# Kernel tuning notes

Measured on AMD Instinct MI355X. Metric: run time of the kernel, lower is better.

The kernel has to match this reference:

```python
import jax, jax.numpy as jnp
import numpy as np

B, S, H, D = 8, 4096, 4096, 128
N_MAX = 64          # max_rope_sentences
THETA = 10000.0     # rope_theta
N_SENT = 40         # random sentence ends per sample (+1 forced at last token)


def setup_inputs() -> dict:
    key = jax.random.key(0)
    k0, k1, k2, k3 = jax.random.split(key, 4)
    hidden_states = jax.random.normal(k0, (B, S, H), jnp.float32)
    # sentence-end mask: N_SENT random positions per row + last token always an end
    m = np.zeros((B, S), np.int32)
    for i in range(B):
        pos = np.random.RandomState(i).choice(S - 1, N_SENT, replace=False)
        m[i, pos] = 1
    m[:, -1] = 1
    splitted_mask = jnp.asarray(m)
    scale = 1.0 / np.sqrt(H).astype(np.float32)
    Wq = jax.random.normal(k1, (H, D), jnp.float32) * scale
    Wk = jax.random.normal(k2, (H, D), jnp.float32) * scale
    Wr = jax.random.normal(k3, (H, 1), jnp.float32) * scale
    bq = jnp.zeros((D,), jnp.float32)
    bk = jnp.zeros((D,), jnp.float32)
    br = jnp.zeros((1,), jnp.float32)
    return dict(hidden_states=hidden_states, splitted_mask=splitted_mask,
                Wq=Wq, bq=bq, Wk=Wk, bk=bk, Wr=Wr, br=br)


def _rope(x, cos, sin):
    # x: [B, N, D]; interleaved complex pairs (even=real, odd=imag)
    a, b = x[..., 0::2], x[..., 1::2]
    ra = a * cos - b * sin
    rb = a * sin + b * cos
    return jnp.stack([ra, rb], axis=-1).reshape(x.shape)


def _rewards(hidden_states, splitted_mask, Wq, bq, Wk, bk, Wr, br):
    q_all = hidden_states @ Wq + bq                     # [B,S,D]
    k_all = hidden_states @ Wk + bk                     # [B,S,D]
    v_all = (hidden_states @ Wr + br)[..., 0]           # [B,S]

    mask = splitted_mask > 0                            # [B,S]
    count = mask.sum(axis=1)                            # [B], >=1 by construction
    rank = jnp.cumsum(mask, axis=1) - 1                 # sentence rank per position
    rank = jnp.where(mask, rank, N_MAX)                 # out-of-range -> dropped
    pos = jnp.broadcast_to(jnp.arange(S), (B, S))
    sent_pos = jnp.zeros((B, N_MAX), jnp.int32).at[
        jnp.arange(B)[:, None], rank].set(pos, mode='drop')   # [B,N_MAX]

    vs = jnp.take_along_axis(v_all, sent_pos, axis=1)               # [B,N]
    qs = jnp.take_along_axis(q_all, sent_pos[..., None], axis=1)    # [B,N,D]
    ks = jnp.take_along_axis(k_all, sent_pos[..., None], axis=1)    # [B,N,D]

    # RoPE over sentence rank 0..N_MAX-1
    freqs = 1.0 / (THETA ** (jnp.arange(0, D, 2, dtype=jnp.float32) / D))
    ang = jnp.arange(N_MAX, dtype=jnp.float32)[:, None] * freqs[None, :]
    cos, sin = jnp.cos(ang)[None], jnp.sin(ang)[None]   # [1,N,D/2]
    qs = _rope(qs, cos, sin)
    ks = _rope(ks, cos, sin)

    # query = rotated q of the LAST sentence in each sample
    seq_q = jnp.take_along_axis(qs, (count - 1)[:, None, None], axis=1)[:, 0]  # [B,D]

    # sentence rewards: first = vs[0], rest = successive diffs
    sr = vs - jnp.pad(vs[:, :-1], ((0, 0), (1, 0)))     # [B,N]

    logits = jnp.einsum('bd,bnd->bn', seq_q, ks) / jnp.sqrt(jnp.float32(D))
    valid = jnp.arange(N_MAX)[None, :] < count[:, None]
    logits = jnp.where(valid, logits, -jnp.inf)
    attn = jax.nn.softmax(logits, axis=-1)              # [B,N]
    seq_reward = jnp.sum(attn * sr, axis=-1)            # [B]
    return seq_reward


def reference(hidden_states, splitted_mask, Wq, bq, Wk, bk, Wr, br):
    rewards = _rewards(hidden_states, splitted_mask, Wq, bq, Wk, bk, Wr, br)
    bs = B // 2
    chosen, reject = rewards[:bs], rewards[bs:]
    loss = jnp.mean(-jax.nn.log_sigmoid(chosen - reject))  # penalty_coef = 0
    return loss, rewards
```

## Files before the change

### kernel.cpp

```cpp
#include <hip/hip_runtime.h>
#include <math.h>

#define BB 8
#define SS 4096
#define HH 4096
#define DD 128
#define NMAX 64

__global__ void scan_kernel(const int* __restrict__ mask,
                            int* __restrict__ sent_pos,
                            int* __restrict__ count) {
    int b = blockIdx.x;
    int lane = threadIdx.x;
    int running = 0;
    const int* mrow = mask + (size_t)b * SS;
    for (int base = 0; base < SS; base += 64) {
        int m = (mrow[base + lane] > 0) ? 1 : 0;
        unsigned long long bal = __ballot(m);
        if (m) {
            int r = running + __popcll(bal & ((1ull << lane) - 1ull));
            if (r < NMAX) sent_pos[b * NMAX + r] = base + lane;
        }
        running += __popcll(bal);
    }
    if (lane == 0) count[b] = running > NMAX ? NMAX : running;
}

__global__ void proj_kernel(const float* __restrict__ hs,
                            const float* __restrict__ Wq, const float* __restrict__ bq,
                            const float* __restrict__ Wk, const float* __restrict__ bk,
                            const float* __restrict__ Wr, const float* __restrict__ br,
                            const int* __restrict__ sent_pos, const int* __restrict__ count,
                            float* __restrict__ qrow,
                            float* __restrict__ krows,
                            float* __restrict__ vs) {
    int b = blockIdx.y;
    int j = blockIdx.x;
    int tid = threadIdx.x;
    bool is_q = (j == NMAX);
    int cnt = count[b];
    if (!is_q && j >= cnt) return;

    int row = is_q ? (SS - 1) : sent_pos[b * NMAX + j];
    const float* x = hs + ((size_t)b * SS + (size_t)row) * HH;

    __shared__ float xs[HH];
    __shared__ float4 red[256];
    __shared__ float vred[256];

    for (int i = tid; i < HH / 4; i += 256)
        ((float4*)xs)[i] = ((const float4*)x)[i];
    __syncthreads();

    const float* W = is_q ? Wq : Wk;
    const float* bias = is_q ? bq : bk;

    int d0 = (tid & 31) * 4;
    int h0 = (tid >> 5) * (HH / 8);
    const float* Wp = W + (size_t)h0 * DD + d0;
    float4 acc = make_float4(0.f, 0.f, 0.f, 0.f);
#pragma unroll 4
    for (int h = 0; h < HH / 8; ++h) {
        float xv = xs[h0 + h];
        float4 w = *(const float4*)Wp;
        Wp += DD;
        acc.x += xv * w.x;
        acc.y += xv * w.y;
        acc.z += xv * w.z;
        acc.w += xv * w.w;
    }
    red[tid] = acc;
    __syncthreads();

    if (tid < 32) {
        float4 s = red[tid];
#pragma unroll
        for (int p = 1; p < 8; ++p) {
            float4 o = red[tid + p * 32];
            s.x += o.x; s.y += o.y; s.z += o.z; s.w += o.w;
        }
        int dd = tid * 4;
        float* outp = is_q ? (qrow + b * DD) : (krows + ((size_t)b * NMAX + j) * DD);
        outp[dd + 0] = s.x + bias[dd + 0];
        outp[dd + 1] = s.y + bias[dd + 1];
        outp[dd + 2] = s.z + bias[dd + 2];
        outp[dd + 3] = s.w + bias[dd + 3];
    }

    if (!is_q) {
        float pv = 0.f;
        for (int h = tid; h < HH; h += 256) pv += xs[h] * Wr[h];
        vred[tid] = pv;
        __syncthreads();
        for (int s = 128; s > 0; s >>= 1) {
            if (tid < s) vred[tid] += vred[tid + s];
            __syncthreads();
        }
        if (tid == 0) vs[b * NMAX + j] = vred[0] + br[0];
    }
}

__global__ void finalize_kernel(const float* __restrict__ qrow,
                                const float* __restrict__ krows,
                                const float* __restrict__ vs,
                                const int* __restrict__ count,
                                float* __restrict__ out) {
    __shared__ float sfreq[64];
    __shared__ float qr[BB][DD];
    __shared__ float rew[BB];

    int tid = threadIdx.x;
    if (tid < 64) sfreq[tid] = powf(10000.f, -(float)tid / 64.f);
    __syncthreads();

    int b = tid >> 6;
    int l = tid & 63;
    int cnt = count[b];

    {
        float2 qp = ((const float2*)(qrow + b * DD))[l];
        float s, c;
        sincosf((float)(cnt - 1) * sfreq[l], &s, &c);
        qr[b][2 * l]     = qp.x * c - qp.y * s;
        qr[b][2 * l + 1] = qp.x * s + qp.y * c;
    }
    __syncthreads();

    float lg = -INFINITY;
    if (l < cnt) {
        const float2* kp = (const float2*)(krows + ((size_t)b * NMAX + l) * DD);
        float acc = 0.f;
#pragma unroll 8
        for (int i = 0; i < 64; ++i) {
            float2 kv = kp[i];
            float s, c;
            sincosf((float)l * sfreq[i], &s, &c);
            float kr0 = kv.x * c - kv.y * s;
            float kr1 = kv.x * s + kv.y * c;
            acc += qr[b][2 * i] * kr0 + qr[b][2 * i + 1] * kr1;
        }
        lg = acc * 0.08838834764831845f;
    }

    float m = lg;
#pragma unroll
    for (int off = 32; off > 0; off >>= 1) m = fmaxf(m, __shfl_xor(m, off));
    float e = expf(lg - m);
    float sum = e;
#pragma unroll
    for (int off = 32; off > 0; off >>= 1) sum += __shfl_xor(sum, off);
    float attn = e / sum;

    float vn = 0.f, vp = 0.f;
    if (l < cnt) {
        vn = vs[b * NMAX + l];
        if (l > 0) vp = vs[b * NMAX + l - 1];
    }
    float r = attn * (vn - vp);
#pragma unroll
    for (int off = 32; off > 0; off >>= 1) r += __shfl_xor(r, off);

    if (l == 0) {
        rew[b] = r;
        out[1 + b] = r;
    }
    __syncthreads();

    if (tid == 0) {
        float L = 0.f;
        for (int i = 0; i < BB / 2; ++i) {
            float z = rew[i] - rew[i + BB / 2];
            L += fmaxf(-z, 0.f) + log1pf(expf(-fabsf(z)));
        }
        out[0] = L / (float)(BB / 2);
    }
}

extern "C" void kernel_launch(void* const* d_in, const int* in_sizes, int n_in,
                              void* d_out, int out_size, void* d_ws, size_t ws_size,
                              hipStream_t stream) {
    const float* hs  = (const float*)d_in[0];
    const int*   msk = (const int*)d_in[1];
    const float* Wq  = (const float*)d_in[2];
    const float* bq  = (const float*)d_in[3];
    const float* Wk  = (const float*)d_in[4];
    const float* bk  = (const float*)d_in[5];
    const float* Wr  = (const float*)d_in[6];
    const float* br  = (const float*)d_in[7];
    float* out = (float*)d_out;

    int* sent_pos = (int*)d_ws;
    int* count    = sent_pos + BB * NMAX;
    float* qrow   = (float*)(count + 8);
    float* krows  = qrow + BB * DD;
    float* vsbuf  = krows + (size_t)BB * NMAX * DD;

    scan_kernel<<<BB, 64, 0, stream>>>(msk, sent_pos, count);
    proj_kernel<<<dim3(NMAX + 1, BB), 256, 0, stream>>>(
        hs, Wq, bq, Wk, bk, Wr, br, sent_pos, count, qrow, krows, vsbuf);
    finalize_kernel<<<1, 512, 0, stream>>>(qrow, krows, vsbuf, count, out);
}
```

Baseline: 687.8 us.

## Batch eight gathered rows per block and split hidden dim with atomic accumulation

The projection kernel now handles eight sentence rows per block, so each weight float4 loaded from Wq/Wk is reused across eight rows instead of one. The hidden dimension is also split into four slices across blockIdx.z, and partial sums are combined with atomicAdd into outputs that are first initialised with the biases. The scan kernel becomes a 256-thread block prefix sum using vectorised mask loads. This cuts the repeated streaming of the 2 MB weight matrices per row and adds parallelism, at the cost of float atomics, which make the summation order nondeterministic, and more registers for the eight accumulators.

```diff
diff --git a/kernel.cpp b/kernel.cpp
--- a/kernel.cpp
+++ b/kernel.cpp
@@ -6,97 +6,160 @@
 #define HH 4096
 #define DD 128
 #define NMAX 64
+#define RPB 8
+#define HSL 1024
 
 __global__ void scan_kernel(const int* __restrict__ mask,
+                            const float* __restrict__ bq,
+                            const float* __restrict__ bk,
+                            const float* __restrict__ br,
                             int* __restrict__ sent_pos,
-                            int* __restrict__ count) {
-    int b = blockIdx.x;
-    int lane = threadIdx.x;
-    int running = 0;
-    const int* mrow = mask + (size_t)b * SS;
-    for (int base = 0; base < SS; base += 64) {
-        int m = (mrow[base + lane] > 0) ? 1 : 0;
-        unsigned long long bal = __ballot(m);
-        if (m) {
-            int r = running + __popcll(bal & ((1ull << lane) - 1ull));
-            if (r < NMAX) sent_pos[b * NMAX + r] = base + lane;
-        }
-        running += __popcll(bal);
-    }
-    if (lane == 0) count[b] = running > NMAX ? NMAX : running;
-}
-
-__global__ void proj_kernel(const float* __restrict__ hs,
-                            const float* __restrict__ Wq, const float* __restrict__ bq,
-                            const float* __restrict__ Wk, const float* __restrict__ bk,
-                            const float* __restrict__ Wr, const float* __restrict__ br,
-                            const int* __restrict__ sent_pos, const int* __restrict__ count,
+                            int* __restrict__ count,
                             float* __restrict__ qrow,
                             float* __restrict__ krows,
                             float* __restrict__ vs) {
+    int b = blockIdx.x;
+    int t = threadIdx.x;
+
+    for (int i = t; i < DD; i += 256) qrow[b * DD + i] = bq[i];
+    for (int i = t; i < NMAX * DD; i += 256) krows[b * NMAX * DD + i] = bk[i & (DD - 1)];
+    if (t < NMAX) vs[b * NMAX + t] = br[0];
+
+    const int4* m4 = (const int4*)(mask + (size_t)b * SS);
+    int vals[16];
+    {
+        int4 v0 = m4[t * 4 + 0], v1 = m4[t * 4 + 1], v2 = m4[t * 4 + 2], v3 = m4[t * 4 + 3];
+        vals[0] = v0.x; vals[1] = v0.y; vals[2] = v0.z; vals[3] = v0.w;
+        vals[4] = v1.x; vals[5] = v1.y; vals[6] = v1.z; vals[7] = v1.w;
+        vals[8] = v2.x; vals[9] = v2.y; vals[10] = v2.z; vals[11] = v2.w;
+        vals[12] = v3.x; vals[13] = v3.y; vals[14] = v3.z; vals[15] = v3.w;
+    }
+    int c = 0;
+#pragma unroll
+    for (int i = 0; i < 16; ++i) c += (vals[i] > 0) ? 1 : 0;
+
+    __shared__ int sc[256];
+    sc[t] = c;
+    __syncthreads();
+    for (int off = 1; off < 256; off <<= 1) {
+        int add = (t >= off) ? sc[t - off] : 0;
+        __syncthreads();
+        sc[t] += add;
+        __syncthreads();
+    }
+    int prefix = sc[t] - c;
+    int total = sc[255];
+
+    int r = prefix;
+#pragma unroll
+    for (int i = 0; i < 16; ++i) {
+        if (vals[i] > 0) {
+            if (r < NMAX) sent_pos[b * NMAX + r] = t * 16 + i;
+            r++;
+        }
+    }
+    if (t == 0) count[b] = total > NMAX ? NMAX : total;
+}
+
+__global__ void __launch_bounds__(256)
+proj_kernel(const float* __restrict__ hs,
+            const float* __restrict__ Wq,
+            const float* __restrict__ Wk,
+            const float* __restrict__ Wr,
+            const int* __restrict__ sent_pos, const int* __restrict__ count,
+            float* __restrict__ qrow,
+            float* __restrict__ krows,
+            float* __restrict__ vs) {
+    int g = blockIdx.x;
     int b = blockIdx.y;
-    int j = blockIdx.x;
-    int tid = threadIdx.x;
-    bool is_q = (j == NMAX);
+    int s = blockIdx.z;
+    int t = threadIdx.x;
     int cnt = count[b];
-    if (!is_q && j >= cnt) return;
-
-    int row = is_q ? (SS - 1) : sent_pos[b * NMAX + j];
-    const float* x = hs + ((size_t)b * SS + (size_t)row) * HH;
-
-    __shared__ float xs[HH];
-    __shared__ float4 red[256];
-    __shared__ float vred[256];
-
-    for (int i = tid; i < HH / 4; i += 256)
-        ((float4*)xs)[i] = ((const float4*)x)[i];
-    __syncthreads();
-
-    const float* W = is_q ? Wq : Wk;
-    const float* bias = is_q ? bq : bk;
-
-    int d0 = (tid & 31) * 4;
-    int h0 = (tid >> 5) * (HH / 8);
-    const float* Wp = W + (size_t)h0 * DD + d0;
-    float4 acc = make_float4(0.f, 0.f, 0.f, 0.f);
-#pragma unroll 4
-    for (int h = 0; h < HH / 8; ++h) {
-        float xv = xs[h0 + h];
-        float4 w = *(const float4*)Wp;
-        Wp += DD;
-        acc.x += xv * w.x;
-        acc.y += xv * w.y;
-        acc.z += xv * w.z;
-        acc.w += xv * w.w;
-    }
-    red[tid] = acc;
-    __syncthreads();
-
-    if (tid < 32) {
-        float4 s = red[tid];
-#pragma unroll
-        for (int p = 1; p < 8; ++p) {
-            float4 o = red[tid + p * 32];
-            s.x += o.x; s.y += o.y; s.z += o.z; s.w += o.w;
-        }
-        int dd = tid * 4;
-        float* outp = is_q ? (qrow + b * DD) : (krows + ((size_t)b * NMAX + j) * DD);
-        outp[dd + 0] = s.x + bias[dd + 0];
-        outp[dd + 1] = s.y + bias[dd + 1];
-        outp[dd + 2] = s.z + bias[dd + 2];
-        outp[dd + 3] = s.w + bias[dd + 3];
-    }
-
-    if (!is_q) {
-        float pv = 0.f;
-        for (int h = tid; h < HH; h += 256) pv += xs[h] * Wr[h];
-        vred[tid] = pv;
-        __syncthreads();
-        for (int s = 128; s > 0; s >>= 1) {
-            if (tid < s) vred[tid] += vred[tid + s];
-            __syncthreads();
-        }
-        if (tid == 0) vs[b * NMAX + j] = vred[0] + br[0];
+    int slot0 = g * RPB;
+    bool is_q_grp = (g == 8);
+    if (!is_q_grp && slot0 >= cnt) return;
+
+    int hoff = s * HSL;
+
+    __shared__ float xs[RPB][HSL];
+    __shared__ float wsum[RPB][4];
+
+    int wv = t >> 6;
+    int lane = t & 63;
+
+    float4 wr = ((const float4*)(Wr + hoff))[t];
+
+    for (int r = 0; r < RPB; ++r) {
+        int slot = slot0 + r;
+        bool valid = is_q_grp ? (r == 0) : (slot < cnt);
+        int row = is_q_grp ? (SS - 1) : (valid ? sent_pos[b * NMAX + slot] : 0);
+        float4 xv = make_float4(0.f, 0.f, 0.f, 0.f);
+        if (valid) {
+            const float4* xp = (const float4*)(hs + ((size_t)b * SS + (size_t)row) * HH + hoff);
+            xv = xp[t];
+        }
+        ((float4*)xs[r])[t] = xv;
+        if (!is_q_grp) {
+            float d = xv.x * wr.x + xv.y * wr.y + xv.z * wr.z + xv.w * wr.w;
+#pragma unroll
+            for (int off = 32; off > 0; off >>= 1) d += __shfl_down(d, off);
+            if (lane == 0) wsum[r][wv] = d;
+        }
+    }
+    __syncthreads();
+
+    if (!is_q_grp && t < RPB) {
+        int slot = slot0 + t;
+        if (slot < cnt)
+            atomicAdd(&vs[b * NMAX + slot], wsum[t][0] + wsum[t][1] + wsum[t][2] + wsum[t][3]);
+    }
+
+    const float* W = is_q_grp ? Wq : Wk;
+    int lane_d = (t & 31) * 4;
+    int hbase = (t >> 5) * (HSL / 8);
+    const float4* wp = (const float4*)(W + (size_t)(hoff + hbase) * DD + lane_d);
+    float4 acc[RPB];
+#pragma unroll
+    for (int r = 0; r < RPB; ++r) acc[r] = make_float4(0.f, 0.f, 0.f, 0.f);
+
+    for (int hl = 0; hl < HSL / 8; ++hl) {
+        float4 w = *wp;
+        wp += DD / 4;
+#pragma unroll
+        for (int r = 0; r < RPB; ++r) {
+            float xv = xs[r][hbase + hl];
+            acc[r].x += xv * w.x;
+            acc[r].y += xv * w.y;
+            acc[r].z += xv * w.z;
+            acc[r].w += xv * w.w;
+        }
+    }
+    __syncthreads();
+
+    float4* red = (float4*)&xs[0][0];
+#pragma unroll
+    for (int r = 0; r < RPB; ++r) red[r * 256 + t] = acc[r];
+    __syncthreads();
+
+    {
+        int r = t >> 5;
+        int dl = t & 31;
+        int slot = slot0 + r;
+        bool valid = is_q_grp ? (r == 0) : (slot < cnt);
+        if (valid) {
+            float4 ssum = red[r * 256 + dl];
+#pragma unroll
+            for (int p = 1; p < 8; ++p) {
+                float4 o = red[r * 256 + p * 32 + dl];
+                ssum.x += o.x; ssum.y += o.y; ssum.z += o.z; ssum.w += o.w;
+            }
+            float* outp = is_q_grp ? (qrow + b * DD + dl * 4)
+                                   : (krows + ((size_t)b * NMAX + slot) * DD + dl * 4);
+            atomicAdd(outp + 0, ssum.x);
+            atomicAdd(outp + 1, ssum.y);
+            atomicAdd(outp + 2, ssum.z);
+            atomicAdd(outp + 3, ssum.w);
+        }
     }
 }
 
@@ -195,8 +258,8 @@
     float* krows  = qrow + BB * DD;
     float* vsbuf  = krows + (size_t)BB * NMAX * DD;
 
-    scan_kernel<<<BB, 64, 0, stream>>>(msk, sent_pos, count);
-    proj_kernel<<<dim3(NMAX + 1, BB), 256, 0, stream>>>(
-        hs, Wq, bq, Wk, bk, Wr, br, sent_pos, count, qrow, krows, vsbuf);
+    scan_kernel<<<BB, 256, 0, stream>>>(msk, bq, bk, br, sent_pos, count, qrow, krows, vsbuf);
+    proj_kernel<<<dim3(9, BB, HH / HSL), 256, 0, stream>>>(
+        hs, Wq, Wk, Wr, sent_pos, count, qrow, krows, vsbuf);
     finalize_kernel<<<1, 512, 0, stream>>>(qrow, krows, vsbuf, count, out);
 }
```

New measurement: 616.5 us. 1.12x faster.
